# Performance work log

Measured on AMD Instinct MI355X. Metric: run time of the kernel, lower is better.

## Reference

```python
import jax, jax.numpy as jnp
import numpy as np

B, L, D = 2, 8192, 1024


def setup_inputs() -> dict:
    key = jax.random.key(0)
    ks = jax.random.split(key, 6)
    x = jax.random.normal(ks[0], (B, L, D), dtype=jnp.float32)
    # phazor param init (torch): exp(2j*pi*arange(D)/D) * |randn(D)|
    mag = jnp.abs(jax.random.normal(ks[1], (D,), dtype=jnp.float32))
    ang = (2.0 * np.pi * jnp.arange(D) / D).astype(jnp.float32)
    phazor_real = mag * jnp.cos(ang)
    phazor_imag = mag * jnp.sin(ang)
    # phazor_init ~ complex randn
    phazor_init_real = jax.random.normal(ks[2], (D,), dtype=jnp.float32)
    phazor_init_imag = jax.random.normal(ks[3], (D,), dtype=jnp.float32)
    # last_conv_init ~ complex randn (first-call hidden state, broadcast over batch)
    last_conv_real = jax.random.normal(ks[4], (D,), dtype=jnp.float32)
    last_conv_imag = jax.random.normal(ks[5], (D,), dtype=jnp.float32)
    return {
        "x": x,
        "phazor_real": phazor_real, "phazor_imag": phazor_imag,
        "phazor_init_real": phazor_init_real, "phazor_init_imag": phazor_init_imag,
        "last_conv_real": last_conv_real, "last_conv_imag": last_conv_imag,
    }


def reference(x, phazor_real, phazor_imag, phazor_init_real, phazor_init_imag,
              last_conv_real, last_conv_imag):
    b, length, dim = x.shape
    dtype = x.dtype
    # reparameterized decay: magnitude exp(-|p|^2), keep angle of p
    ph = jnp.exp(-(phazor_real * phazor_real + phazor_imag * phazor_imag)) \
         * jnp.exp(1j * jnp.arctan2(phazor_imag, phazor_real))          # [D] complex
    # phazor_progression[t, d] = ph[d] ** t
    prog = jnp.power(ph[None, :], jnp.arange(length)[:, None])           # [L, D]
    pinit = phazor_init_real + 1j * phazor_init_imag                     # [D]
    filt = prog * pinit[None, :]                                         # [L, D]
    # FFT convolution with zero-padding to 2L (linear convolution)
    filt_fft = jnp.fft.fft(filt, n=2 * length, axis=0)                   # [2L, D]
    x_fft = jnp.fft.fft(x.astype(jnp.complex64), n=2 * length, axis=1)   # [B, 2L, D]
    conv = jnp.fft.ifft(filt_fft[None, :, :] * x_fft, axis=1)[:, :length, :]  # [B, L, D]
    # carry in hidden state from previous chunk (here: learned init, broadcast over batch)
    last = (last_conv_real + 1j * last_conv_imag)[None, None, :]          # [1, 1, D]
    conv_with_past = conv + last * prog[None, :, :] * ph[None, None, :]
    return conv_with_past.real.astype(dtype)
```

## Files before the change

kernel.cpp:

```cpp
#include <hip/hip_runtime.h>

#define BB 2
#define LL 8192
#define DD 1024
#define NC 64
#define TT 128
#define NPAIR (DD/2)
#define FOLD_BATCH 16

__device__ __forceinline__ void compute_ph(float pr, float pi, float& phr, float& phi) {
    float r2 = fmaf(pr, pr, pi * pi);
    float mag = expf(-r2);
    float r = sqrtf(r2);
    if (r > 1e-30f) {
        float inv = mag / r;
        phr = pr * inv;
        phi = pi * inv;
    } else {
        phr = mag;
        phi = 0.0f;
    }
}

#define LD8(buf, g) \
    { _Pragma("unroll") for (int u = 0; u < 8; ++u) \
        buf[u] = xp[(size_t)((g) * 8 + u) * NPAIR]; }

#define CP8P(buf) \
    { _Pragma("unroll") for (int u = 0; u < 8; ++u) { \
        float2 xv = buf[u]; \
        float nr0 = fmaf(phr0, s0r, fmaf(-phi0, s0i, q0r * xv.x)); \
        float ni0 = fmaf(phi0, s0r, fmaf( phr0, s0i, q0i * xv.x)); \
        float nr1 = fmaf(phr1, s1r, fmaf(-phi1, s1i, q1r * xv.y)); \
        float ni1 = fmaf(phi1, s1r, fmaf( phr1, s1i, q1i * xv.y)); \
        s0r = nr0; s0i = ni0; s1r = nr1; s1i = ni1; } }

#define CP8F(buf) \
    { _Pragma("unroll") for (int u = 0; u < 8; ++u) { \
        float2 xv = buf[u]; \
        float nr0 = fmaf(phr0, s0r, fmaf(-phi0, s0i, q0r * xv.x)); \
        float ni0 = fmaf(phi0, s0r, fmaf( phr0, s0i, q0i * xv.x)); \
        float nr1 = fmaf(phr1, s1r, fmaf(-phi1, s1i, q1r * xv.y)); \
        float ni1 = fmaf(phi1, s1r, fmaf( phr1, s1i, q1i * xv.y)); \
        s0r = nr0; s0i = ni0; s1r = nr1; s1i = ni1; \
        buf[u] = make_float2(nr0, nr1); } }

#define ST8(buf, g) \
    { _Pragma("unroll") for (int u = 0; u < 8; ++u) \
        op[(size_t)((g) * 8 + u) * NPAIR] = buf[u]; }

__global__ __launch_bounds__(256) void k_partial(
    const float* __restrict__ x,
    const float* __restrict__ pr, const float* __restrict__ pi,
    const float* __restrict__ qr, const float* __restrict__ qi,
    float4* __restrict__ partial)
{
    const int p = blockIdx.x * 256 + threadIdx.x;
    const int j = blockIdx.y;
    const int b = blockIdx.z;
    const int d0 = 2 * p, d1 = d0 + 1;

    float phr0, phi0, phr1, phi1;
    compute_ph(pr[d0], pi[d0], phr0, phi0);
    compute_ph(pr[d1], pi[d1], phr1, phi1);
    const float q0r = qr[d0], q0i = qi[d0], q1r = qr[d1], q1i = qi[d1];

    const float2* xp = (const float2*)(x + ((size_t)b * LL + (size_t)j * TT) * DD) + p;

    float s0r = 0.f, s0i = 0.f, s1r = 0.f, s1i = 0.f;
    float2 bufA[8], bufB[8];
    LD8(bufA, 0);  LD8(bufB, 1);
    CP8P(bufA);    LD8(bufA, 2);
    CP8P(bufB);    LD8(bufB, 3);
    CP8P(bufA);    LD8(bufA, 4);
    CP8P(bufB);    LD8(bufB, 5);
    CP8P(bufA);    LD8(bufA, 6);
    CP8P(bufB);    LD8(bufB, 7);
    CP8P(bufA);    LD8(bufA, 8);
    CP8P(bufB);    LD8(bufB, 9);
    CP8P(bufA);    LD8(bufA, 10);
    CP8P(bufB);    LD8(bufB, 11);
    CP8P(bufA);    LD8(bufA, 12);
    CP8P(bufB);    LD8(bufB, 13);
    CP8P(bufA);    LD8(bufA, 14);
    CP8P(bufB);    LD8(bufB, 15);
    CP8P(bufA);
    CP8P(bufB);

    partial[((size_t)b * NC + j) * NPAIR + p] = make_float4(s0r, s0i, s1r, s1i);
}

__global__ __launch_bounds__(256) void k_final(
    const float* __restrict__ x,
    const float* __restrict__ pr, const float* __restrict__ pi,
    const float* __restrict__ qr, const float* __restrict__ qi,
    const float* __restrict__ lr, const float* __restrict__ li,
    const float4* __restrict__ partial,
    float* __restrict__ out)
{
    const int p = blockIdx.x * 256 + threadIdx.x;
    const int j = blockIdx.y;
    const int b = blockIdx.z;
    const int d0 = 2 * p, d1 = d0 + 1;

    float phr0, phi0, phr1, phi1;
    compute_ph(pr[d0], pi[d0], phr0, phi0);
    compute_ph(pr[d1], pi[d1], phr1, phi1);
    const float q0r = qr[d0], q0i = qi[d0], q1r = qr[d1], q1i = qi[d1];

    float a0r = phr0, a0i = phi0, a1r = phr1, a1i = phi1;
    #pragma unroll
    for (int k = 0; k < 7; ++k) {
        float n0r = a0r * a0r - a0i * a0i, n0i = 2.f * a0r * a0i;
        float n1r = a1r * a1r - a1i * a1i, n1i = 2.f * a1r * a1i;
        a0r = n0r; a0i = n0i; a1r = n1r; a1i = n1i;
    }

    float s0r = lr[d0], s0i = li[d0], s1r = lr[d1], s1i = li[d1];
    const float4* pb = partial + (size_t)b * NC * NPAIR + p;
    for (int bs = 0; bs < j; bs += FOLD_BATCH) {
        float4 buf[FOLD_BATCH];
        #pragma unroll
        for (int u = 0; u < FOLD_BATCH; ++u) {
            int k = bs + u;
            int kc = (k < j) ? k : (j - 1);
            buf[u] = pb[(size_t)kc * NPAIR];
        }
        #pragma unroll
        for (int u = 0; u < FOLD_BATCH; ++u) {
            int k = bs + u;
            if (k < j) {
                float n0r = fmaf(a0r, s0r, fmaf(-a0i, s0i, buf[u].x));
                float n0i = fmaf(a0i, s0r, fmaf( a0r, s0i, buf[u].y));
                float n1r = fmaf(a1r, s1r, fmaf(-a1i, s1i, buf[u].z));
                float n1i = fmaf(a1i, s1r, fmaf( a1r, s1i, buf[u].w));
                s0r = n0r; s0i = n0i; s1r = n1r; s1i = n1i;
            }
        }
    }

    const size_t rowbase = (size_t)b * LL + (size_t)j * TT;
    const float2* xp = (const float2*)(x + rowbase * DD) + p;
    float2* op = (float2*)(out + rowbase * DD) + p;

    float2 bufA[8], bufB[8];
    LD8(bufA, 0);  LD8(bufB, 1);
    CP8F(bufA);  ST8(bufA, 0);  LD8(bufA, 2);
    CP8F(bufB);  ST8(bufB, 1);  LD8(bufB, 3);
    CP8F(bufA);  ST8(bufA, 2);  LD8(bufA, 4);
    CP8F(bufB);  ST8(bufB, 3);  LD8(bufB, 5);
    CP8F(bufA);  ST8(bufA, 4);  LD8(bufA, 6);
    CP8F(bufB);  ST8(bufB, 5);  LD8(bufB, 7);
    CP8F(bufA);  ST8(bufA, 6);  LD8(bufA, 8);
    CP8F(bufB);  ST8(bufB, 7);  LD8(bufB, 9);
    CP8F(bufA);  ST8(bufA, 8);  LD8(bufA, 10);
    CP8F(bufB);  ST8(bufB, 9);  LD8(bufB, 11);
    CP8F(bufA);  ST8(bufA, 10); LD8(bufA, 12);
    CP8F(bufB);  ST8(bufB, 11); LD8(bufB, 13);
    CP8F(bufA);  ST8(bufA, 12); LD8(bufA, 14);
    CP8F(bufB);  ST8(bufB, 13); LD8(bufB, 15);
    CP8F(bufA);  ST8(bufA, 14);
    CP8F(bufB);  ST8(bufB, 15);
}

extern "C" void kernel_launch(void* const* d_in, const int* in_sizes, int n_in,
                              void* d_out, int out_size, void* d_ws, size_t ws_size,
                              hipStream_t stream) {
    const float* x  = (const float*)d_in[0];
    const float* pr = (const float*)d_in[1];
    const float* pi = (const float*)d_in[2];
    const float* qr = (const float*)d_in[3];
    const float* qi = (const float*)d_in[4];
    const float* lr = (const float*)d_in[5];
    const float* li = (const float*)d_in[6];
    float* out = (float*)d_out;

    float4* partial = (float4*)d_ws;

    dim3 grid(NPAIR / 256, NC, BB);
    k_partial<<<grid, 256, 0, stream>>>(x, pr, pi, qr, qi, partial);
    k_final<<<grid, 256, 0, stream>>>(x, pr, pi, qr, qi, lr, li, partial, out);
}
```

Measured before the change: 40.06 us.

## Halve chunk length and add hierarchical two-level carry aggregation kernel

Chunks shrink from 128 to 64 timesteps, doubling the number of chunks and the blocks in each kernel. A new k_agg kernel folds groups of 8 chunk partials into 16 group carries, so k_final folds at most 16 group carries plus up to 7 chunk partials instead of up to 63 partials serially. This shortens the serial carry chain and raises parallelism, at the cost of an extra launch and more partial-state traffic.

```diff
diff --git a/kernel.cpp b/kernel.cpp
--- a/kernel.cpp
+++ b/kernel.cpp
@@ -3,10 +3,11 @@
 #define BB 2
 #define LL 8192
 #define DD 1024
-#define NC 64
-#define TT 128
+#define NC 128
+#define TT 64
+#define NG 16
+#define GSZ 8
 #define NPAIR (DD/2)
-#define FOLD_BATCH 16
 
 __device__ __forceinline__ void compute_ph(float pr, float pi, float& phr, float& phi) {
     float r2 = fmaf(pr, pr, pi * pi);
@@ -49,6 +50,15 @@
     { _Pragma("unroll") for (int u = 0; u < 8; ++u) \
         op[(size_t)((g) * 8 + u) * NPAIR] = buf[u]; }
 
+#define FOLD0(ar_, ai_, vr, vi) \
+    { float nr = fmaf(ar_, s0r, fmaf(-(ai_), s0i, vr)); \
+      float ni = fmaf(ai_, s0r, fmaf( (ar_), s0i, vi)); \
+      s0r = nr; s0i = ni; }
+#define FOLD1(ar_, ai_, vr, vi) \
+    { float nr = fmaf(ar_, s1r, fmaf(-(ai_), s1i, vr)); \
+      float ni = fmaf(ai_, s1r, fmaf( (ar_), s1i, vi)); \
+      s1r = nr; s1i = ni; }
+
 __global__ __launch_bounds__(256) void k_partial(
     const float* __restrict__ x,
     const float* __restrict__ pr, const float* __restrict__ pi,
@@ -76,18 +86,47 @@
     CP8P(bufB);    LD8(bufB, 5);
     CP8P(bufA);    LD8(bufA, 6);
     CP8P(bufB);    LD8(bufB, 7);
-    CP8P(bufA);    LD8(bufA, 8);
-    CP8P(bufB);    LD8(bufB, 9);
-    CP8P(bufA);    LD8(bufA, 10);
-    CP8P(bufB);    LD8(bufB, 11);
-    CP8P(bufA);    LD8(bufA, 12);
-    CP8P(bufB);    LD8(bufB, 13);
-    CP8P(bufA);    LD8(bufA, 14);
-    CP8P(bufB);    LD8(bufB, 15);
     CP8P(bufA);
     CP8P(bufB);
 
     partial[((size_t)b * NC + j) * NPAIR + p] = make_float4(s0r, s0i, s1r, s1i);
+}
+
+__global__ __launch_bounds__(256) void k_agg(
+    const float* __restrict__ pr, const float* __restrict__ pi,
+    const float4* __restrict__ partial,
+    float4* __restrict__ Q)
+{
+    const int idx = blockIdx.x * 256 + threadIdx.x;
+    const int p = idx & (NPAIR - 1);
+    const int rest = idx >> 9;
+    const int g = rest & (NG - 1);
+    const int b = rest >> 4;
+    const int d0 = 2 * p, d1 = d0 + 1;
+
+    float phr0, phi0, phr1, phi1;
+    compute_ph(pr[d0], pi[d0], phr0, phi0);
+    compute_ph(pr[d1], pi[d1], phr1, phi1);
+    float a0r = phr0, a0i = phi0, a1r = phr1, a1i = phi1;
+    #pragma unroll
+    for (int k = 0; k < 6; ++k) {
+        float n0r = a0r*a0r - a0i*a0i, n0i = 2.f*a0r*a0i;
+        float n1r = a1r*a1r - a1i*a1i, n1i = 2.f*a1r*a1i;
+        a0r = n0r; a0i = n0i; a1r = n1r; a1i = n1i;
+    }
+
+    const float4* pb = partial + ((size_t)b * NC + (size_t)g * GSZ) * NPAIR + p;
+    float4 Pm[GSZ];
+    #pragma unroll
+    for (int m = 0; m < GSZ; ++m) Pm[m] = pb[(size_t)m * NPAIR];
+
+    float s0r = 0.f, s0i = 0.f, s1r = 0.f, s1i = 0.f;
+    #pragma unroll
+    for (int m = 0; m < GSZ; ++m) {
+        FOLD0(a0r, a0i, Pm[m].x, Pm[m].y)
+        FOLD1(a1r, a1i, Pm[m].z, Pm[m].w)
+    }
+    Q[((size_t)b * NG + g) * NPAIR + p] = make_float4(s0r, s0i, s1r, s1i);
 }
 
 __global__ __launch_bounds__(256) void k_final(
@@ -96,12 +135,15 @@
     const float* __restrict__ qr, const float* __restrict__ qi,
     const float* __restrict__ lr, const float* __restrict__ li,
     const float4* __restrict__ partial,
+    const float4* __restrict__ Q,
     float* __restrict__ out)
 {
     const int p = blockIdx.x * 256 + threadIdx.x;
     const int j = blockIdx.y;
     const int b = blockIdx.z;
     const int d0 = 2 * p, d1 = d0 + 1;
+    const int g = j >> 3;
+    const int r = j & 7;
 
     float phr0, phi0, phr1, phi1;
     compute_ph(pr[d0], pi[d0], phr0, phi0);
@@ -110,31 +152,51 @@
 
     float a0r = phr0, a0i = phi0, a1r = phr1, a1i = phi1;
     #pragma unroll
-    for (int k = 0; k < 7; ++k) {
-        float n0r = a0r * a0r - a0i * a0i, n0i = 2.f * a0r * a0i;
-        float n1r = a1r * a1r - a1i * a1i, n1i = 2.f * a1r * a1i;
+    for (int k = 0; k < 6; ++k) {
+        float n0r = a0r*a0r - a0i*a0i, n0i = 2.f*a0r*a0i;
+        float n1r = a1r*a1r - a1i*a1i, n1i = 2.f*a1r*a1i;
         a0r = n0r; a0i = n0i; a1r = n1r; a1i = n1i;
     }
+    float A0r = a0r, A0i = a0i, A1r = a1r, A1i = a1i;
+    #pragma unroll
+    for (int k = 0; k < 3; ++k) {
+        float n0r = A0r*A0r - A0i*A0i, n0i = 2.f*A0r*A0i;
+        float n1r = A1r*A1r - A1i*A1i, n1i = 2.f*A1r*A1i;
+        A0r = n0r; A0i = n0i; A1r = n1r; A1i = n1i;
+    }
 
     float s0r = lr[d0], s0i = li[d0], s1r = lr[d1], s1i = li[d1];
-    const float4* pb = partial + (size_t)b * NC * NPAIR + p;
-    for (int bs = 0; bs < j; bs += FOLD_BATCH) {
-        float4 buf[FOLD_BATCH];
-        #pragma unroll
-        for (int u = 0; u < FOLD_BATCH; ++u) {
-            int k = bs + u;
-            int kc = (k < j) ? k : (j - 1);
+
+    if (g > 0) {
+        const float4* qb = Q + (size_t)b * NG * NPAIR + p;
+        float4 buf[16];
+        #pragma unroll
+        for (int u = 0; u < 16; ++u) {
+            int kc = (u < g) ? u : 0;
+            buf[u] = qb[(size_t)kc * NPAIR];
+        }
+        #pragma unroll
+        for (int u = 0; u < 16; ++u) {
+            if (u < g) {
+                FOLD0(A0r, A0i, buf[u].x, buf[u].y)
+                FOLD1(A1r, A1i, buf[u].z, buf[u].w)
+            }
+        }
+    }
+
+    if (r > 0) {
+        const float4* pb = partial + ((size_t)b * NC + (size_t)g * GSZ) * NPAIR + p;
+        float4 buf[8];
+        #pragma unroll
+        for (int u = 0; u < 8; ++u) {
+            int kc = (u < r) ? u : 0;
             buf[u] = pb[(size_t)kc * NPAIR];
         }
         #pragma unroll
-        for (int u = 0; u < FOLD_BATCH; ++u) {
-            int k = bs + u;
-            if (k < j) {
-                float n0r = fmaf(a0r, s0r, fmaf(-a0i, s0i, buf[u].x));
-                float n0i = fmaf(a0i, s0r, fmaf( a0r, s0i, buf[u].y));
-                float n1r = fmaf(a1r, s1r, fmaf(-a1i, s1i, buf[u].z));
-                float n1i = fmaf(a1i, s1r, fmaf( a1r, s1i, buf[u].w));
-                s0r = n0r; s0i = n0i; s1r = n1r; s1i = n1i;
+        for (int u = 0; u < 8; ++u) {
+            if (u < r) {
+                FOLD0(a0r, a0i, buf[u].x, buf[u].y)
+                FOLD1(a1r, a1i, buf[u].z, buf[u].w)
             }
         }
     }
@@ -151,16 +213,8 @@
     CP8F(bufB);  ST8(bufB, 3);  LD8(bufB, 5);
     CP8F(bufA);  ST8(bufA, 4);  LD8(bufA, 6);
     CP8F(bufB);  ST8(bufB, 5);  LD8(bufB, 7);
-    CP8F(bufA);  ST8(bufA, 6);  LD8(bufA, 8);
-    CP8F(bufB);  ST8(bufB, 7);  LD8(bufB, 9);
-    CP8F(bufA);  ST8(bufA, 8);  LD8(bufA, 10);
-    CP8F(bufB);  ST8(bufB, 9);  LD8(bufB, 11);
-    CP8F(bufA);  ST8(bufA, 10); LD8(bufA, 12);
-    CP8F(bufB);  ST8(bufB, 11); LD8(bufB, 13);
-    CP8F(bufA);  ST8(bufA, 12); LD8(bufA, 14);
-    CP8F(bufB);  ST8(bufB, 13); LD8(bufB, 15);
-    CP8F(bufA);  ST8(bufA, 14);
-    CP8F(bufB);  ST8(bufB, 15);
+    CP8F(bufA);  ST8(bufA, 6);
+    CP8F(bufB);  ST8(bufB, 7);
 }
 
 extern "C" void kernel_launch(void* const* d_in, const int* in_sizes, int n_in,
@@ -176,8 +230,10 @@
     float* out = (float*)d_out;
 
     float4* partial = (float4*)d_ws;
+    float4* Q       = partial + (size_t)BB * NC * NPAIR;
 
     dim3 grid(NPAIR / 256, NC, BB);
     k_partial<<<grid, 256, 0, stream>>>(x, pr, pi, qr, qi, partial);
-    k_final<<<grid, 256, 0, stream>>>(x, pr, pi, qr, qi, lr, li, partial, out);
-}
+    k_agg<<<(BB * NG * NPAIR) / 256, 256, 0, stream>>>(pr, pi, partial, Q);
+    k_final<<<grid, 256, 0, stream>>>(x, pr, pi, qr, qi, lr, li, partial, Q, out);
+}
```

Measured after the change: 43.50 us. 1.09x slower.

## Process one channel per thread in final pass to double parallelism

Applied to the files above, without the earlier changes.

The final kernel now gives each thread a single channel instead of a pair, doubling its grid and using scalar float loads and stores in place of float2. The partial-state buffer is re-laid out per channel as float2, so the final pass reads 8-byte values while the partial kernel still writes paired float4s. The aim is more waves in flight to hide memory latency and the serial recurrence. In exchange, phase and decay setup and the carry fold are repeated per channel, and each memory access is narrower.

```diff
diff --git a/kernel.cpp b/kernel.cpp
--- a/kernel.cpp
+++ b/kernel.cpp
@@ -35,25 +35,27 @@
         float ni1 = fmaf(phi1, s1r, fmaf( phr1, s1i, q1i * xv.y)); \
         s0r = nr0; s0i = ni0; s1r = nr1; s1i = ni1; } }
 
-#define CP8F(buf) \
+#define SLD8(buf, g) \
+    { _Pragma("unroll") for (int u = 0; u < 8; ++u) \
+        buf[u] = xp[(size_t)((g) * 8 + u) * DD]; }
+
+#define SCP8F(buf) \
     { _Pragma("unroll") for (int u = 0; u < 8; ++u) { \
-        float2 xv = buf[u]; \
-        float nr0 = fmaf(phr0, s0r, fmaf(-phi0, s0i, q0r * xv.x)); \
-        float ni0 = fmaf(phi0, s0r, fmaf( phr0, s0i, q0i * xv.x)); \
-        float nr1 = fmaf(phr1, s1r, fmaf(-phi1, s1i, q1r * xv.y)); \
-        float ni1 = fmaf(phi1, s1r, fmaf( phr1, s1i, q1i * xv.y)); \
-        s0r = nr0; s0i = ni0; s1r = nr1; s1i = ni1; \
-        buf[u] = make_float2(nr0, nr1); } }
+        float xv = buf[u]; \
+        float nr = fmaf(phr, sr, fmaf(-phi, si, qre * xv)); \
+        float ni = fmaf(phi, sr, fmaf( phr, si, qim * xv)); \
+        sr = nr; si = ni; \
+        buf[u] = nr; } }
 
-#define ST8(buf, g) \
+#define SST8(buf, g) \
     { _Pragma("unroll") for (int u = 0; u < 8; ++u) \
-        op[(size_t)((g) * 8 + u) * NPAIR] = buf[u]; }
+        op[(size_t)((g) * 8 + u) * DD] = buf[u]; }
 
 __global__ __launch_bounds__(256) void k_partial(
     const float* __restrict__ x,
     const float* __restrict__ pr, const float* __restrict__ pi,
     const float* __restrict__ qr, const float* __restrict__ qi,
-    float4* __restrict__ partial)
+    float2* __restrict__ partial)
 {
     const int p = blockIdx.x * 256 + threadIdx.x;
     const int j = blockIdx.y;
@@ -87,7 +89,8 @@
     CP8P(bufA);
     CP8P(bufB);
 
-    partial[((size_t)b * NC + j) * NPAIR + p] = make_float4(s0r, s0i, s1r, s1i);
+    float4* pp = (float4*)(partial + ((size_t)b * NC + j) * DD + d0);
+    *pp = make_float4(s0r, s0i, s1r, s1i);
 }
 
 __global__ __launch_bounds__(256) void k_final(
@@ -95,72 +98,67 @@
     const float* __restrict__ pr, const float* __restrict__ pi,
     const float* __restrict__ qr, const float* __restrict__ qi,
     const float* __restrict__ lr, const float* __restrict__ li,
-    const float4* __restrict__ partial,
+    const float2* __restrict__ partial,
     float* __restrict__ out)
 {
-    const int p = blockIdx.x * 256 + threadIdx.x;
+    const int d = blockIdx.x * 256 + threadIdx.x;
     const int j = blockIdx.y;
     const int b = blockIdx.z;
-    const int d0 = 2 * p, d1 = d0 + 1;
 
-    float phr0, phi0, phr1, phi1;
-    compute_ph(pr[d0], pi[d0], phr0, phi0);
-    compute_ph(pr[d1], pi[d1], phr1, phi1);
-    const float q0r = qr[d0], q0i = qi[d0], q1r = qr[d1], q1i = qi[d1];
+    float phr, phi; compute_ph(pr[d], pi[d], phr, phi);
+    const float qre = qr[d], qim = qi[d];
 
-    float a0r = phr0, a0i = phi0, a1r = phr1, a1i = phi1;
+    float ar = phr, ai = phi;
     #pragma unroll
     for (int k = 0; k < 7; ++k) {
-        float n0r = a0r * a0r - a0i * a0i, n0i = 2.f * a0r * a0i;
-        float n1r = a1r * a1r - a1i * a1i, n1i = 2.f * a1r * a1i;
-        a0r = n0r; a0i = n0i; a1r = n1r; a1i = n1i;
+        float nr = ar * ar - ai * ai;
+        float ni = 2.f * ar * ai;
+        ar = nr; ai = ni;
     }
 
-    float s0r = lr[d0], s0i = li[d0], s1r = lr[d1], s1i = li[d1];
-    const float4* pb = partial + (size_t)b * NC * NPAIR + p;
+    float sr = lr[d], si = li[d];
+    const float2* pb = partial + (size_t)b * NC * DD + d;
     for (int bs = 0; bs < j; bs += FOLD_BATCH) {
-        float4 buf[FOLD_BATCH];
+        float2 buf[FOLD_BATCH];
         #pragma unroll
         for (int u = 0; u < FOLD_BATCH; ++u) {
             int k = bs + u;
             int kc = (k < j) ? k : (j - 1);
-            buf[u] = pb[(size_t)kc * NPAIR];
+            buf[u] = pb[(size_t)kc * DD];
         }
         #pragma unroll
         for (int u = 0; u < FOLD_BATCH; ++u) {
             int k = bs + u;
             if (k < j) {
-                float n0r = fmaf(a0r, s0r, fmaf(-a0i, s0i, buf[u].x));
-                float n0i = fmaf(a0i, s0r, fmaf( a0r, s0i, buf[u].y));
-                float n1r = fmaf(a1r, s1r, fmaf(-a1i, s1i, buf[u].z));
-                float n1i = fmaf(a1i, s1r, fmaf( a1r, s1i, buf[u].w));
-                s0r = n0r; s0i = n0i; s1r = n1r; s1i = n1i;
+                float nr = fmaf(ar, sr, fmaf(-ai, si, buf[u].x));
+                float ni = fmaf(ai, sr, fmaf( ar, si, buf[u].y));
+                sr = nr; si = ni;
             }
         }
     }
 
-    const size_t rowbase = (size_t)b * LL + (size_t)j * TT;
-    const float2* xp = (const float2*)(x + rowbase * DD) + p;
-    float2* op = (float2*)(out + rowbase * DD) + p;
+    const size_t base = ((size_t)b * LL + (size_t)j * TT) * DD + d;
+    const float* xp = x + base;
+    float* op = out + base;
 
-    float2 bufA[8], bufB[8];
-    LD8(bufA, 0);  LD8(bufB, 1);
-    CP8F(bufA);  ST8(bufA, 0);  LD8(bufA, 2);
-    CP8F(bufB);  ST8(bufB, 1);  LD8(bufB, 3);
-    CP8F(bufA);  ST8(bufA, 2);  LD8(bufA, 4);
-    CP8F(bufB);  ST8(bufB, 3);  LD8(bufB, 5);
-    CP8F(bufA);  ST8(bufA, 4);  LD8(bufA, 6);
-    CP8F(bufB);  ST8(bufB, 5);  LD8(bufB, 7);
-    CP8F(bufA);  ST8(bufA, 6);  LD8(bufA, 8);
-    CP8F(bufB);  ST8(bufB, 7);  LD8(bufB, 9);
-    CP8F(bufA);  ST8(bufA, 8);  LD8(bufA, 10);
-    CP8F(bufB);  ST8(bufB, 9);  LD8(bufB, 11);
-    CP8F(bufA);  ST8(bufA, 10); LD8(bufA, 12);
-    CP8F(bufB);  ST8(bufB, 11); LD8(bufB, 13);
-    CP8F(bufA);  ST8(bufA, 12); LD8(bufA, 14);
-    CP8F(bufB);  ST8(bufB, 13); LD8(bufB, 15);
-    CP8F(bufA);  ST8(bufA, 14);
-    CP8F(bufB);  ST8(bufB, 15);
+    float bufA[8], bufB[8];
+    SLD8(bufA, 0);  SLD8(bufB, 1);
+    SCP8F(bufA);  SST8(bufA, 0);  SLD8(bufA, 2);
+    SCP8F(bufB);  SST8(bufB, 1);  SLD8(bufB, 3);
+    SCP8F(bufA);  SST8(bufA, 2);  SLD8(bufA, 4);
+    SCP8F(bufB);  SST8(bufB, 3);  SLD8(bufB, 5);
+    SCP8F(bufA);  SST8(bufA, 4);  SLD8(bufA, 6);
+    SCP8F(bufB);  SST8(bufB, 5);  SLD8(bufB, 7);
+    SCP8F(bufA);  SST8(bufA, 6);  SLD8(bufA, 8);
+    SCP8F(bufB);  SST8(bufB, 7);  SLD8(bufB, 9);
+    SCP8F(bufA);  SST8(bufA, 8);  SLD8(bufA, 10);
+    SCP8F(bufB);  SST8(bufB, 9);  SLD8(bufB, 11);
+    SCP8F(bufA);  SST8(bufA, 10); SLD8(bufA, 12);
+    SCP8F(bufB);  SST8(bufB, 11); SLD8(bufB, 13);
+    SCP8F(bufA);  SST8(bufA, 12); SLD8(bufA, 14);
+    SCP8F(bufB);  SST8(bufB, 13); SLD8(bufB, 15);
+    SCP8F(bufA);  SST8(bufA, 14);
+    SCP8F(bufB);  SST8(bufB, 15);
 }
 
 extern "C" void kernel_launch(void* const* d_in, const int* in_sizes, int n_in,
@@ -175,9 +173,10 @@
     const float* li = (const float*)d_in[6];
     float* out = (float*)d_out;
 
-    float4* partial = (float4*)d_ws;
+    float2* partial = (float2*)d_ws;
 
-    dim3 grid(NPAIR / 256, NC, BB);
-    k_partial<<<grid, 256, 0, stream>>>(x, pr, pi, qr, qi, partial);
-    k_final<<<grid, 256, 0, stream>>>(x, pr, pi, qr, qi, lr, li, partial, out);
+    dim3 grid1(NPAIR / 256, NC, BB);
+    dim3 grid2(DD / 256, NC, BB);
+    k_partial<<<grid1, 256, 0, stream>>>(x, pr, pi, qr, qi, partial);
+    k_final<<<grid2, 256, 0, stream>>>(x, pr, pi, qr, qi, lr, li, partial, out);
 }
```

Result: no change. 40.65 us (+1.5%).
